# Kernel optimization log

Hardware: AMD Instinct MI355X
Metric: run time of the kernel (lower is better)

## Reference

```python
import jax, jax.numpy as jnp
import numpy as np

NHEADS = 4   # attention heads (search_cfg.nheads)
WS = 7       # spatial search window side -> WS*WS candidates per query
PS = 3       # patch size for distance computation (search_cfg.ps)
K = 16       # top-k neighbors kept (search_cfg.k)


def layer_norm_2d(vid, w, b, eps=1e-6):
    # LayerNorm over channel dim at every (t,h,w) location; vid (B,T,C,H,W)
    mu = vid.mean(axis=2, keepdims=True)
    var = vid.var(axis=2, keepdims=True)
    y = (vid - mu) / jnp.sqrt(var + eps)
    return y * w[None, None, :, None, None] + b[None, None, :, None, None]


def conv1x1(vid, w, b):
    # 1x1 ConvQKV projection: vid (B,T,C,H,W), w (O,C)
    return jnp.einsum('btchw,oc->btohw', vid, w) + b[None, None, :, None, None]


def box_sum(x, ps):
    # sum over centered ps x ps patch (zero pad); x (..., H, W)
    r = ps // 2
    H, W = x.shape[-2], x.shape[-1]
    xp = jnp.pad(x, [(0, 0)] * (x.ndim - 2) + [(r, r), (r, r)])
    out = jnp.zeros_like(x)
    ah, aw = x.ndim - 2, x.ndim - 1
    for dy in range(ps):
        for dx in range(ps):
            s = jax.lax.dynamic_slice_in_dim(xp, dy, H, ah)
            s = jax.lax.dynamic_slice_in_dim(s, dx, W, aw)
            out = out + s
    return out


def nl_search(q, k):
    # patch-based non-local search: q,k (B,T,HD,c,H,W)
    B, T, HD, c, H, W = q.shape
    r = WS // 2
    kp = jnp.pad(k, ((0, 0),) * 4 + ((r, r), (r, r)))  # zero pad = invalid candidates score ~0
    offs = jnp.stack(jnp.meshgrid(jnp.arange(WS), jnp.arange(WS), indexing='ij'), -1).reshape(-1, 2)

    @jax.checkpoint
    def step(carry, off):
        dy, dx = off[0], off[1]
        ksh = jax.lax.dynamic_slice(kp, (0, 0, 0, 0, dy, dx), (B, T, HD, c, H, W))
        s = (q * ksh).sum(axis=3)      # pixel inner products (B,T,HD,H,W)
        s = box_sum(s, PS)             # patch inner products
        return carry, s

    _, scores = jax.lax.scan(step, 0, offs)        # (WS*WS,B,T,HD,H,W)
    scores = jnp.moveaxis(scores, 0, -1)           # (B,T,HD,H,W,WS*WS)
    dists, inds = jax.lax.top_k(scores, K)         # top-k neighbors per query
    return dists, inds


def nl_stack(v, weights, inds):
    # gather the K selected neighbor values, weighted; v (B,T,HD,c,H,W)
    B, T, HD, c, H, W = v.shape
    r = WS // 2
    vp = jnp.pad(v, ((0, 0),) * 4 + ((r, r), (r, r)))
    Hp, Wp = H + 2 * r, W + 2 * r
    row = jnp.arange(H)[:, None, None] + inds // WS   # (B,T,HD,H,W,K)
    col = jnp.arange(W)[None, :, None] + inds % WS
    lin = (row * Wp + col).reshape(B, T, HD, 1, H * W * K)
    vf = vp.reshape(B, T, HD, c, Hp * Wp)
    g = jnp.take_along_axis(vf, jnp.broadcast_to(lin, (B, T, HD, c, H * W * K)), axis=-1)
    g = g.reshape(B, T, HD, c, H, W, K)
    g = g * weights[:, :, :, None]                    # weight each neighbor
    # -> (B*T, HD*c, K, H, W) stack for Conv3d projection
    return jnp.transpose(g, (0, 1, 2, 3, 6, 4, 5)).reshape(B * T, HD * c, K, H, W)


def proj3d(stack, w, b):
    # Conv3d(io_dim, io_dim, (K,3,3), stride=(K,1,1), pad=(0,1,1), groups=NHEADS)
    out = jax.lax.conv_general_dilated(
        stack, w, window_strides=(K, 1, 1),
        padding=((0, 0), (1, 1), (1, 1)),
        dimension_numbers=('NCDHW', 'OIDHW', 'NCDHW'),
        feature_group_count=NHEADS)
    return out[:, :, 0] + b[None, :, None, None]


def setup_inputs() -> dict:
    key = jax.random.key(0)
    ks = jax.random.split(key, 8)
    B, T, C, H, W = 1, 4, 128, 96, 96
    sc = 1.0 / np.sqrt(C)
    inp = {
        'vid': jax.random.normal(ks[0], (B, T, C, H, W), jnp.float32),
        'ln_w': jnp.ones((C,), jnp.float32),
        'ln_b': jnp.zeros((C,), jnp.float32),
        'wq': jax.random.normal(ks[1], (C, C), jnp.float32) * sc,
        'bq': jnp.zeros((C,), jnp.float32),
        'wk': jax.random.normal(ks[2], (C, C), jnp.float32) * sc,
        'bk': jnp.zeros((C,), jnp.float32),
        'wv': jax.random.normal(ks[3], (C, C), jnp.float32) * sc,
        'bv': jnp.zeros((C,), jnp.float32),
        'proj_w': jax.random.normal(ks[4], (C, C // NHEADS, K, 3, 3), jnp.float32) * 0.02,
        'proj_b': jnp.zeros((C,), jnp.float32),
    }
    return inp


def reference(vid, ln_w, ln_b, wq, bq, wk, bk, wv, bv, proj_w, proj_b):
    B, T, C, H, W = vid.shape
    x = layer_norm_2d(vid, ln_w, ln_b)
    q = conv1x1(x, wq, bq)
    k = conv1x1(x, wk, bk)
    v = conv1x1(x, wv, bv)
    hd = lambda t: t.reshape(B, T, NHEADS, C // NHEADS, H, W)
    q, k, v = hd(q), hd(k), hd(v)
    dists, inds = nl_search(q, k)                 # k-NN search
    weights = jax.nn.softmax(dists, axis=-1)      # normalize over K
    stack = nl_stack(v, weights, inds)            # neighbor stacking
    out = proj3d(stack, proj_w, proj_b)           # conv projection collapses K
    return out.reshape(B, T, C, H, W)
```

## Files before the change

kernel.cpp:

```cpp
#include <hip/hip_runtime.h>


typedef float  f32x4  __attribute__((ext_vector_type(4)));
typedef __bf16 bf16x8 __attribute__((ext_vector_type(8)));
typedef __bf16 bf16x4 __attribute__((ext_vector_type(4)));

__device__ __forceinline__ float dpp_shr1(float x) {
  return __int_as_float(__builtin_amdgcn_update_dpp(0, __float_as_int(x), 0x111, 0xf, 0xf, false));
}
__device__ __forceinline__ float dpp_shl1(float x) {
  return __int_as_float(__builtin_amdgcn_update_dpp(0, __float_as_int(x), 0x101, 0xf, 0xf, false));
}

__global__ __launch_bounds__(256) void prep_kernel(
    const float* __restrict__ wq, const float* __restrict__ wk, const float* __restrict__ wv,
    const float* __restrict__ pw, float* __restrict__ Wt, __bf16* __restrict__ pwt) {
  int idx = blockIdx.x * 256 + threadIdx.x;
  const int NPW = 4 * 16 * 9 * 32 * 32;
  if (idx < NPW) {
    int i  = idx & 31;
    int ol = (idx >> 5) & 31;
    int d  = (idx >> 10) % 9;
    int r  = (idx >> 10) / 9;
    int kd = r & 15;
    int g  = r >> 4;
    int o  = g * 32 + ol;
    pwt[idx] = (__bf16)pw[((o * 32 + i) * 16 + kd) * 9 + d];
  } else {
    int widx = idx - NPW;
    if (widx < 128 * 384) {
      int o = widx % 384;
      int c = widx / 384;
      const float* __restrict__ src = (o < 128) ? wq : (o < 256 ? wk : wv);
      Wt[widx] = src[(o & 127) * 128 + c];
    }
  }
}

__global__ __launch_bounds__(64) void ln_stats_kernel(
    const float* __restrict__ vid, float* __restrict__ mu, float* __restrict__ rs) {
  int pix = blockIdx.x * 64 + threadIdx.x;
  int f = blockIdx.y;
  const float* __restrict__ vp = vid + (size_t)f * 128 * 9216 + pix;
  float s = 0.f, s2 = 0.f;
  #pragma unroll 8
  for (int c = 0; c < 128; ++c) { float x = vp[(size_t)c * 9216]; s += x; s2 += x * x; }
  float m_ = s * (1.f / 128.f);
  float v_ = fmaxf(s2 * (1.f / 128.f) - m_ * m_, 0.f);
  mu[f * 9216 + pix] = m_;
  rs[f * 9216 + pix] = rsqrtf(v_ + 1e-6f);
}

__global__ __launch_bounds__(512) void qkv_gemm_kernel(
    const float* __restrict__ vid, const float* __restrict__ mu, const float* __restrict__ rs,
    const float* __restrict__ lnw, const float* __restrict__ lnb,
    const float* __restrict__ Wt, const float* __restrict__ bq, const float* __restrict__ bk,
    const float* __restrict__ bv, float* __restrict__ qb, float* __restrict__ kb,
    __bf16* __restrict__ vbbf) {
  __shared__ __align__(16) float Xs[32][128];
  __shared__ __align__(16) float Ws[32][128];
  __shared__ float muL[128], rsL[128], lwS[128], lbS[128];
  int tid = threadIdx.x;
  int mt = blockIdx.y;
  int N0 = blockIdx.x * 128;
  int f  = mt / 72;
  int pf = (mt % 72) * 128;

  if (tid < 128) {
    muL[tid] = mu[f * 9216 + pf + tid];
    rsL[tid] = rs[f * 9216 + pf + tid];
  } else if (tid < 256) {
    int t2 = tid - 128;
    lwS[t2] = lnw[t2];
    lbS[t2] = lnb[t2];
  }

  int tx = tid & 15, ty = tid >> 4;
  int m0 = ty * 4;
  int sm = tid & 127;
  int sk = tid >> 7;
  float acc[4][8];
  #pragma unroll
  for (int a = 0; a < 4; ++a)
    #pragma unroll
    for (int b = 0; b < 8; ++b) acc[a][b] = 0.f;

  const size_t vbase = (size_t)f * 128 * 9216 + pf;
  float xr[8], wr[8];

  #pragma unroll
  for (int it = 0; it < 8; ++it) {
    int kk = sk + 4 * it;
    xr[it] = vid[vbase + (size_t)kk * 9216 + sm];
    wr[it] = Wt[(size_t)kk * 384 + N0 + sm];
  }
  __syncthreads();
  #pragma unroll
  for (int it = 0; it < 8; ++it) {
    int kk = sk + 4 * it;
    Xs[kk][sm] = (xr[it] - muL[sm]) * rsL[sm] * lwS[kk] + lbS[kk];
    Ws[kk][sm] = wr[it];
  }
  __syncthreads();

  for (int kc = 0; kc < 4; ++kc) {
    if (kc < 3) {
      #pragma unroll
      for (int it = 0; it < 8; ++it) {
        int kk = sk + 4 * it;
        int c = (kc + 1) * 32 + kk;
        xr[it] = vid[vbase + (size_t)c * 9216 + sm];
        wr[it] = Wt[(size_t)c * 384 + N0 + sm];
      }
    }
    #pragma unroll 4
    for (int kk = 0; kk < 32; ++kk) {
      float xa[4], wa[8];
      *(float4*)&xa[0] = *(const float4*)&Xs[kk][m0];
      *(float4*)&wa[0] = *(const float4*)&Ws[kk][tx * 4];
      *(float4*)&wa[4] = *(const float4*)&Ws[kk][64 + tx * 4];
      #pragma unroll
      for (int a = 0; a < 4; ++a)
        #pragma unroll
        for (int b = 0; b < 8; ++b)
          acc[a][b] = fmaf(xa[a], wa[b], acc[a][b]);
    }
    if (kc < 3) {
      __syncthreads();
      #pragma unroll
      for (int it = 0; it < 8; ++it) {
        int kk = sk + 4 * it;
        int c = (kc + 1) * 32 + kk;
        Xs[kk][sm] = (xr[it] - muL[sm]) * rsL[sm] * lwS[c] + lbS[c];
        Ws[kk][sm] = wr[it];
      }
      __syncthreads();
    }
  }

  int sel = blockIdx.x;
  int nlo = tx * 4, nhi = 64 + tx * 4;
  int hlo = nlo >> 5, clo = nlo & 31;
  int hhi = nhi >> 5, chi = nhi & 31;
  const float* __restrict__ bias = (sel == 0) ? bq : (sel == 1 ? bk : bv);
  float4 blo = make_float4(bias[nlo], bias[nlo + 1], bias[nlo + 2], bias[nlo + 3]);
  float4 bhi = make_float4(bias[nhi], bias[nhi + 1], bias[nhi + 2], bias[nhi + 3]);
  size_t base_lo = (size_t)(f * 4 + hlo) * 9216 * 32 + clo;
  size_t base_hi = (size_t)(f * 4 + hhi) * 9216 * 32 + chi;
  if (sel < 2) {
    float* __restrict__ dst = (sel == 0) ? qb : kb;
    #pragma unroll
    for (int a = 0; a < 4; ++a) {
      size_t poff = (size_t)(pf + m0 + a) * 32;
      *(float4*)&dst[base_lo + poff] = make_float4(acc[a][0] + blo.x, acc[a][1] + blo.y,
                                                   acc[a][2] + blo.z, acc[a][3] + blo.w);
      *(float4*)&dst[base_hi + poff] = make_float4(acc[a][4] + bhi.x, acc[a][5] + bhi.y,
                                                   acc[a][6] + bhi.z, acc[a][7] + bhi.w);
    }
  } else {
    #pragma unroll
    for (int a = 0; a < 4; ++a) {
      size_t poff = (size_t)(pf + m0 + a) * 32;
      bf16x4 lo4, hi4;
      lo4[0] = (__bf16)(acc[a][0] + blo.x); lo4[1] = (__bf16)(acc[a][1] + blo.y);
      lo4[2] = (__bf16)(acc[a][2] + blo.z); lo4[3] = (__bf16)(acc[a][3] + blo.w);
      hi4[0] = (__bf16)(acc[a][4] + bhi.x); hi4[1] = (__bf16)(acc[a][5] + bhi.y);
      hi4[2] = (__bf16)(acc[a][6] + bhi.z); hi4[3] = (__bf16)(acc[a][7] + bhi.w);
      *(bf16x4*)&vbbf[base_lo + poff] = lo4;
      *(bf16x4*)&vbbf[base_hi + poff] = hi4;
    }
  }
}

__global__ __launch_bounds__(256, 3) void search_kernel(
    const float* __restrict__ qb, const float* __restrict__ kb,
    float* __restrict__ wgtb, int* __restrict__ indb) {
  __shared__ __align__(16) float klds[16 * 22 * 32];
  __shared__ float slds[7][256];
  int tid = threadIdx.x;
  int th = blockIdx.y;
  int tile = blockIdx.x;
  int iy0 = (tile / 7) * 14, ix0 = (tile % 7) * 14;
  const float* __restrict__ kbase = kb + (size_t)th * 9216 * 32;

  #pragma unroll
  for (int it = 0; it < 11; ++it) {
    int i = it * 256 + tid;
    int r = i / 176, rem = i % 176;
    int col = rem >> 3, c4 = rem & 7;
    int gy = iy0 - 4 + r, gx = ix0 - 4 + col;
    float4 val = make_float4(0.f, 0.f, 0.f, 0.f);
    if ((unsigned)gy < 96u && (unsigned)gx < 96u)
      val = *(const float4*)&kbase[(size_t)(gy * 96 + gx) * 32 + c4 * 4];
    int p = r * 22 + col;
    *(float4*)&klds[p * 32 + ((c4 ^ (p & 7)) << 2)] = val;
  }

  int sy = tid >> 4, sx = tid & 15;
  int qy = iy0 - 1 + sy, qx = ix0 - 1 + sx;
  bool qok = (unsigned)qy < 96u && (unsigned)qx < 96u;
  float4 qv[8];
  #pragma unroll
  for (int j = 0; j < 8; ++j) qv[j] = make_float4(0.f, 0.f, 0.f, 0.f);
  if (qok) {
    const float* __restrict__ qp = qb + ((size_t)th * 9216 + qy * 96 + qx) * 32;
    #pragma unroll
    for (int j = 0; j < 8; ++j) qv[j] = *(const float4*)&qp[j * 4];
  }
  bool inner = (sy >= 1) && (sy <= 14) && (sx >= 1) && (sx <= 14) && qok;

  float tv[16]; int tix[16];
  #pragma unroll
  for (int j = 0; j < 16; ++j) { tv[j] = -3.0e38f; tix[j] = 0; }
  __syncthreads();

  #pragma unroll 1
  for (int dy = 0; dy < 7; ++dy) {
    if (dy > 0) {
      if (tid < 176) {
        int col = tid >> 3, c4 = tid & 7;
        int r = dy + 15;
        int gy = iy0 - 4 + r, gx = ix0 - 4 + col;
        float4 val = make_float4(0.f, 0.f, 0.f, 0.f);
        if ((unsigned)gy < 96u && (unsigned)gx < 96u)
          val = *(const float4*)&kbase[(size_t)(gy * 96 + gx) * 32 + c4 * 4];
        int p = (r & 15) * 22 + col;
        *(float4*)&klds[p * 32 + ((c4 ^ (p & 7)) << 2)] = val;
      }
      __syncthreads();
    }
    float h[7];
    #pragma unroll
    for (int dx = 0; dx < 7; ++dx) {
      int p = ((sy + dy) & 15) * 22 + (sx + dx);
      const float* __restrict__ kp = &klds[p * 32];
      int sw = p & 7;
      float sdot = 0.f;
      #pragma unroll
      for (int j = 0; j < 8; ++j) {
        float4 kq = *(const float4*)&kp[(j ^ sw) << 2];
        sdot += qv[j].x * kq.x + qv[j].y * kq.y + qv[j].z * kq.z + qv[j].w * kq.w;
      }
      h[dx] = sdot + dpp_shr1(sdot) + dpp_shl1(sdot);
      slds[dx][tid] = h[dx];
    }
    __syncthreads();
    if (inner) {
      #pragma unroll
      for (int dx = 0; dx < 7; ++dx) {
        float sc = h[dx] + slds[dx][tid - 16] + slds[dx][tid + 16];
        int oi = dy * 7 + dx;
        float cv = sc; int ci = oi;
        #pragma unroll
        for (int j = 0; j < 16; ++j) {
          bool gt = cv > tv[j];
          float mx = fmaxf(tv[j], cv);
          float mn = fminf(tv[j], cv);
          int nt = gt ? ci : tix[j];
          ci = gt ? tix[j] : ci;
          tv[j] = mx; cv = mn; tix[j] = nt;
        }
      }
    }
  }

  if (inner) {
    float mx = tv[0];
    float e[16], ssum = 0.f;
    #pragma unroll
    for (int j = 0; j < 16; ++j) { e[j] = __expf(tv[j] - mx); ssum += e[j]; }
    float inv = 1.f / ssum;
    size_t base = ((size_t)th * 9216 + qy * 96 + qx) * 16;
    #pragma unroll
    for (int j = 0; j < 4; ++j) {
      *(float4*)&wgtb[base + j * 4] =
          make_float4(e[j*4] * inv, e[j*4+1] * inv, e[j*4+2] * inv, e[j*4+3] * inv);
      *(int4*)&indb[base + j * 4] = make_int4(tix[j*4], tix[j*4+1], tix[j*4+2], tix[j*4+3]);
    }
  }
}

#define STAGE_A(BUF, VR, WC) do {                                              \
  if (gact) {                                                                  \
    __bf16 tmp_[32];                                                           \
    _Pragma("unroll")                                                          \
    for (int wv_ = 0; wv_ < 4; ++wv_) {                                        \
      unsigned uu_[4] = {(unsigned)VR[wv_].x, (unsigned)VR[wv_].y,             \
                         (unsigned)VR[wv_].z, (unsigned)VR[wv_].w};            \
      _Pragma("unroll")                                                        \
      for (int j2_ = 0; j2_ < 4; ++j2_) {                                      \
        float lo_ = __uint_as_float(uu_[j2_] << 16);                           \
        float hi_ = __uint_as_float(uu_[j2_] & 0xffff0000u);                   \
        tmp_[wv_ * 8 + j2_ * 2]     = (__bf16)(lo_ * (WC));                    \
        tmp_[wv_ * 8 + j2_ * 2 + 1] = (__bf16)(hi_ * (WC));                    \
      }                                                                        \
    }                                                                          \
    __bf16* dst_ = &(BUF)[tid * 32];                                           \
    int sela_ = (tid >> 1) & 3;                                                \
    *(int4*)&dst_[(0 ^ sela_) << 3] = *(const int4*)&tmp_[0];                  \
    *(int4*)&dst_[(1 ^ sela_) << 3] = *(const int4*)&tmp_[8];                  \
    *(int4*)&dst_[(2 ^ sela_) << 3] = *(const int4*)&tmp_[16];                 \
    *(int4*)&dst_[(3 ^ sela_) << 3] = *(const int4*)&tmp_[24];                 \
  }                                                                            \
} while (0)

#define STAGE_B(BUF, KD) do {                                                  \
  const __bf16* __restrict__ bsrc_ = pwt + (size_t)(g * 16 + (KD)) * 9216;     \
  _Pragma("unroll")                                                            \
  for (int itb_ = 0; itb_ < 3; ++itb_) {                                       \
    int i_ = itb_ * 512 + tid;                                                 \
    if (i_ < 1152) {                                                           \
      int row_ = i_ >> 2, c_ = i_ & 3;                                         \
      *(int4*)&(BUF)[row_ * 32 + ((c_ ^ ((row_ >> 1) & 3)) << 3)] =            \
          *(const int4*)&bsrc_[row_ * 32 + c_ * 8];                            \
    }                                                                          \
  }                                                                            \
} while (0)

#define GATHER(VR, WC, IND, W) do {                                            \
  int ind_ = (IND);                                                            \
  VR[0] = VR[1] = VR[2] = VR[3] = make_int4(0, 0, 0, 0);                       \
  if (inb) {                                                                   \
    int ny_ = gy + ind_ / 7 - 3, nx_ = gx + ind_ % 7 - 3;                      \
    if ((unsigned)ny_ < 96u && (unsigned)nx_ < 96u) {                          \
      const int4* __restrict__ vp_ =                                           \
          (const int4*)(vbase + (size_t)(ny_ * 96 + nx_) * 32);                \
      VR[0] = vp_[0]; VR[1] = vp_[1]; VR[2] = vp_[2]; VR[3] = vp_[3];          \
    }                                                                          \
  }                                                                            \
  WC = (W);                                                                    \
} while (0)

#define MFMA_PHASE(AB, BB) do {                                                \
  _Pragma("unroll")                                                            \
  for (int dx2_ = 0; dx2_ < 3; ++dx2_) {                                       \
    bf16x8 a_[4];                                                              \
    _Pragma("unroll")                                                          \
    for (int r_ = 0; r_ < 4; ++r_) {                                           \
      int p_ = (wid * 2 + r_) * 18 + lr + dx2_;                                \
      a_[r_] = *(const bf16x8*)&(AB)[p_ * 32 + ((kg ^ ((p_ >> 1) & 3)) << 3)]; \
    }                                                                          \
    _Pragma("unroll")                                                          \
    for (int dy2_ = 0; dy2_ < 3; ++dy2_) {                                     \
      int d_ = dy2_ * 3 + dx2_;                                                \
      bf16x8 b0_ = *(const bf16x8*)&(BB)[(d_ * 32 + lr) * 32 + bswz];          \
      bf16x8 b1_ = *(const bf16x8*)&(BB)[(d_ * 32 + 16 + lr) * 32 + bswz];     \
      acc[0][0] = __builtin_amdgcn_mfma_f32_16x16x32_bf16(a_[dy2_],     b0_, acc[0][0], 0, 0, 0); \
      acc[0][1] = __builtin_amdgcn_mfma_f32_16x16x32_bf16(a_[dy2_],     b1_, acc[0][1], 0, 0, 0); \
      acc[1][0] = __builtin_amdgcn_mfma_f32_16x16x32_bf16(a_[dy2_ + 1], b0_, acc[1][0], 0, 0, 0); \
      acc[1][1] = __builtin_amdgcn_mfma_f32_16x16x32_bf16(a_[dy2_ + 1], b1_, acc[1][1], 0, 0, 0); \
    }                                                                          \
  }                                                                            \
} while (0)

__global__ __launch_bounds__(512) void proj_kernel(
    const __bf16* __restrict__ vb, const float* __restrict__ wgtb, const int* __restrict__ indb,
    const __bf16* __restrict__ pwt, const float* __restrict__ pb, float* __restrict__ outp) {
  __shared__ __align__(16) __bf16 Albuf[2][324 * 32];
  __shared__ __align__(16) __bf16 Blbuf[2][288 * 32];
  int tid = threadIdx.x;
  int bid = blockIdx.x;
  int wg = (bid & 7) * 72 + (bid >> 3);
  int th = wg / 36;
  int tile = wg % 36;
  int g = th & 3;
  int ty0 = (tile / 6) * 16, tx0 = (tile % 6) * 16;
  int lane = tid & 63, wid = tid >> 6;
  int kg = lane >> 4, lr = lane & 15;
  int bswz = (kg ^ ((lr >> 1) & 3)) << 3;

  bool gact = tid < 324;
  int ry = tid / 18, rx = tid % 18;
  int gy = ty0 - 1 + ry, gx = tx0 - 1 + rx;
  bool inb = gact && (unsigned)gy < 96u && (unsigned)gx < 96u;
  const __bf16* __restrict__ vbase = vb + (size_t)th * 9216 * 32;
  size_t pxoff = inb ? (size_t)(gy * 96 + gx) : 0;
  const int*   __restrict__ ibase = indb + ((size_t)th * 9216 + pxoff) * 16;
  const float* __restrict__ wbase = wgtb + ((size_t)th * 9216 + pxoff) * 16;

  f32x4 acc[2][2];
  acc[0][0] = (f32x4)(0.0f); acc[0][1] = (f32x4)(0.0f);
  acc[1][0] = (f32x4)(0.0f); acc[1][1] = (f32x4)(0.0f);

  int4 iw_i = make_int4(0, 0, 0, 0);
  float4 iw_w = make_float4(0.f, 0.f, 0.f, 0.f);
  int4 vr0[4], vr1[4];
  float wc0 = 0.f, wc1 = 0.f;

  if (inb) {
    iw_i = *(const int4*)&ibase[0];
    iw_w = *(const float4*)&wbase[0];
  }
  GATHER(vr0, wc0, iw_i.x, iw_w.x);
  STAGE_A(Albuf[0], vr0, wc0);
  STAGE_B(Blbuf[0], 0);
  GATHER(vr1, wc1, iw_i.y, iw_w.y);
  __syncthreads();

  #pragma unroll 1
  for (int kq = 0; kq < 4; ++kq) {
    int k4 = kq * 4;
    STAGE_A(Albuf[1], vr1, wc1);
    STAGE_B(Blbuf[1], k4 + 1);
    GATHER(vr0, wc0, iw_i.z, iw_w.z);
    MFMA_PHASE(Albuf[0], Blbuf[0]);
    __syncthreads();
    STAGE_A(Albuf[0], vr0, wc0);
    STAGE_B(Blbuf[0], k4 + 2);
    GATHER(vr1, wc1, iw_i.w, iw_w.w);
    MFMA_PHASE(Albuf[1], Blbuf[1]);
    __syncthreads();
    STAGE_A(Albuf[1], vr1, wc1);
    STAGE_B(Blbuf[1], k4 + 3);
    if (kq < 3) {
      if (inb) {
        iw_i = *(const int4*)&ibase[k4 + 4];
        iw_w = *(const float4*)&wbase[k4 + 4];
      }
      GATHER(vr0, wc0, iw_i.x, iw_w.x);
    }
    MFMA_PHASE(Albuf[0], Blbuf[0]);
    __syncthreads();
    if (kq < 3) {
      STAGE_A(Albuf[0], vr0, wc0);
      STAGE_B(Blbuf[0], k4 + 4);
      GATHER(vr1, wc1, iw_i.y, iw_w.y);
    }
    MFMA_PHASE(Albuf[1], Blbuf[1]);
    __syncthreads();
  }

  int x0 = tx0 + kg * 4;
  int f = th >> 2;
  #pragma unroll
  for (int mt = 0; mt < 2; ++mt) {
    int y = ty0 + wid * 2 + mt;
    #pragma unroll
    for (int nt = 0; nt < 2; ++nt) {
      int o = g * 32 + nt * 16 + lr;
      float bias = pb[o];
      float4 res = make_float4(acc[mt][nt][0] + bias, acc[mt][nt][1] + bias,
                               acc[mt][nt][2] + bias, acc[mt][nt][3] + bias);
      *(float4*)&outp[(size_t)(f * 128 + o) * 9216 + y * 96 + x0] = res;
    }
  }
}

extern "C" void kernel_launch(void* const* d_in, const int* in_sizes, int n_in,
                              void* d_out, int out_size, void* d_ws, size_t ws_size,
                              hipStream_t stream) {
  const float* vid = (const float*)d_in[0];
  const float* lnw = (const float*)d_in[1];
  const float* lnb = (const float*)d_in[2];
  const float* wq  = (const float*)d_in[3];
  const float* bq  = (const float*)d_in[4];
  const float* wk  = (const float*)d_in[5];
  const float* bk  = (const float*)d_in[6];
  const float* wv_ = (const float*)d_in[7];
  const float* bv  = (const float*)d_in[8];
  const float* pw  = (const float*)d_in[9];
  const float* pb  = (const float*)d_in[10];
  float* outp = (float*)d_out;

  const size_t SZ_T  = (size_t)16 * 9216 * 32 * 4;
  const size_t SZ_TB = (size_t)16 * 9216 * 32 * 2;
  const size_t SZ_W  = (size_t)16 * 9216 * 16 * 4;
  const size_t SZ_WT = 128 * 384 * 4;
  const size_t SZ_PW = (size_t)4 * 16 * 9 * 32 * 32 * 2;
  const size_t SZ_MU = (size_t)4 * 9216 * 4;

  char* p = (char*)d_ws;
  float* qb = (float*)p;        p += SZ_T;
  float* kb = (float*)p;        p += SZ_T;
  __bf16* vbbf = (__bf16*)p;    p += SZ_TB;
  float* wgtb = (float*)p;      p += SZ_W;
  int*   indb = (int*)p;        p += SZ_W;
  float* Wt = (float*)p;        p += SZ_WT;
  __bf16* pwt = (__bf16*)p;     p += SZ_PW;
  float* mu = (float*)p;        p += SZ_MU;
  float* rs = (float*)p;

  prep_kernel<<<2496, 256, 0, stream>>>(wq, wk, wv_, pw, Wt, pwt);
  ln_stats_kernel<<<dim3(144, 4), 64, 0, stream>>>(vid, mu, rs);
  qkv_gemm_kernel<<<dim3(3, 288), 512, 0, stream>>>(vid, mu, rs, lnw, lnb, Wt, bq, bk, bv,
                                                    qb, kb, vbbf);
  search_kernel<<<dim3(49, 16), 256, 0, stream>>>(qb, kb, wgtb, indb);
  proj_kernel<<<576, 512, 0, stream>>>(vbbf, wgtb, indb, pwt, pb, outp);
}
```

Measured before the change: 209.9 us.

## Compute V projection with bf16 MFMA from a precomputed normalized bf16 input

The V third of the fp32 QKV GEMM is split out. A new kernel writes the layer-normalized input as channel-contiguous bf16, and a new kernel computes V with bf16 MFMA instructions using swizzled LDS tiles. Q and K stay on the existing fp32 GEMM, which now runs two column blocks instead of three. This moves V onto matrix cores, at the cost of two extra launches, an extra bf16 buffer written and read through global memory, and lower precision in the V inputs.

```diff
diff --git a/kernel.cpp b/kernel.cpp
--- a/kernel.cpp
+++ b/kernel.cpp
@@ -3,7 +3,6 @@
 
 typedef float  f32x4  __attribute__((ext_vector_type(4)));
 typedef __bf16 bf16x8 __attribute__((ext_vector_type(8)));
-typedef __bf16 bf16x4 __attribute__((ext_vector_type(4)));
 
 __device__ __forceinline__ float dpp_shr1(float x) {
   return __int_as_float(__builtin_amdgcn_update_dpp(0, __float_as_int(x), 0x111, 0xf, 0xf, false));
@@ -14,7 +13,8 @@
 
 __global__ __launch_bounds__(256) void prep_kernel(
     const float* __restrict__ wq, const float* __restrict__ wk, const float* __restrict__ wv,
-    const float* __restrict__ pw, float* __restrict__ Wt, __bf16* __restrict__ pwt) {
+    const float* __restrict__ pw, float* __restrict__ Wt, __bf16* __restrict__ pwt,
+    __bf16* __restrict__ wvh) {
   int idx = blockIdx.x * 256 + threadIdx.x;
   const int NPW = 4 * 16 * 9 * 32 * 32;
   if (idx < NPW) {
@@ -26,14 +26,15 @@
     int g  = r >> 4;
     int o  = g * 32 + ol;
     pwt[idx] = (__bf16)pw[((o * 32 + i) * 16 + kd) * 9 + d];
+  } else if (idx < NPW + 128 * 384) {
+    int widx = idx - NPW;
+    int o = widx % 384;
+    int c = widx / 384;
+    const float* __restrict__ src = (o < 128) ? wq : (o < 256 ? wk : wv);
+    Wt[widx] = src[(o & 127) * 128 + c];
   } else {
-    int widx = idx - NPW;
-    if (widx < 128 * 384) {
-      int o = widx % 384;
-      int c = widx / 384;
-      const float* __restrict__ src = (o < 128) ? wq : (o < 256 ? wk : wv);
-      Wt[widx] = src[(o & 127) * 128 + c];
-    }
+    int vidx = idx - NPW - 128 * 384;
+    if (vidx < 128 * 128) wvh[vidx] = (__bf16)wv[vidx];
   }
 }
 
@@ -51,12 +52,47 @@
   rs[f * 9216 + pix] = rsqrtf(v_ + 1e-6f);
 }
 
-__global__ __launch_bounds__(512) void qkv_gemm_kernel(
+__global__ __launch_bounds__(256) void xbf_kernel(
+    const float* __restrict__ vid, const float* __restrict__ mu, const float* __restrict__ rs,
+    const float* __restrict__ lnw, const float* __restrict__ lnb, __bf16* __restrict__ xbf) {
+  __shared__ __align__(16) __bf16 tile[128 * 128];
+  __shared__ float muL[128], rsL[128], lwS[128], lbS[128];
+  int t = threadIdx.x;
+  int pf = blockIdx.x * 128;
+  int f = blockIdx.y;
+  if (t < 128) { muL[t] = mu[f * 9216 + pf + t]; rsL[t] = rs[f * 9216 + pf + t]; }
+  else { lwS[t - 128] = lnw[t - 128]; lbS[t - 128] = lnb[t - 128]; }
+  __syncthreads();
+  #pragma unroll 4
+  for (int it = 0; it < 16; ++it) {
+    int idx = it * 256 + t;
+    int c = idx >> 5, p4 = idx & 31;
+    float4 v = *(const float4*)&vid[((size_t)(f * 128 + c)) * 9216 + pf + p4 * 4];
+    float xs[4] = {v.x, v.y, v.z, v.w};
+    #pragma unroll
+    for (int i = 0; i < 4; ++i) {
+      int pix = p4 * 4 + i;
+      float xn = (xs[i] - muL[pix]) * rsL[pix] * lwS[c] + lbS[c];
+      int cp = c ^ (((pix >> 2) & 7) << 3);
+      tile[pix * 128 + cp] = (__bf16)xn;
+    }
+  }
+  __syncthreads();
+  int pix = t >> 1, half = t & 1;
+  __bf16* __restrict__ dst = xbf + ((size_t)(f * 9216) + pf + pix) * 128 + half * 64;
+  #pragma unroll
+  for (int cc = 0; cc < 8; ++cc) {
+    int chunk = half * 8 + cc;
+    int cs = chunk ^ ((pix >> 2) & 7);
+    *(int4*)&dst[cc * 8] = *(const int4*)&tile[pix * 128 + cs * 8];
+  }
+}
+
+__global__ __launch_bounds__(512) void qk_gemm_kernel(
     const float* __restrict__ vid, const float* __restrict__ mu, const float* __restrict__ rs,
     const float* __restrict__ lnw, const float* __restrict__ lnb,
     const float* __restrict__ Wt, const float* __restrict__ bq, const float* __restrict__ bk,
-    const float* __restrict__ bv, float* __restrict__ qb, float* __restrict__ kb,
-    __bf16* __restrict__ vbbf) {
+    float* __restrict__ qb, float* __restrict__ kb) {
   __shared__ __align__(16) float Xs[32][128];
   __shared__ __align__(16) float Ws[32][128];
   __shared__ float muL[128], rsL[128], lwS[128], lbS[128];
@@ -142,32 +178,91 @@
   int nlo = tx * 4, nhi = 64 + tx * 4;
   int hlo = nlo >> 5, clo = nlo & 31;
   int hhi = nhi >> 5, chi = nhi & 31;
-  const float* __restrict__ bias = (sel == 0) ? bq : (sel == 1 ? bk : bv);
+  const float* __restrict__ bias = (sel == 0) ? bq : bk;
+  float* __restrict__ dst = (sel == 0) ? qb : kb;
   float4 blo = make_float4(bias[nlo], bias[nlo + 1], bias[nlo + 2], bias[nlo + 3]);
   float4 bhi = make_float4(bias[nhi], bias[nhi + 1], bias[nhi + 2], bias[nhi + 3]);
   size_t base_lo = (size_t)(f * 4 + hlo) * 9216 * 32 + clo;
   size_t base_hi = (size_t)(f * 4 + hhi) * 9216 * 32 + chi;
-  if (sel < 2) {
-    float* __restrict__ dst = (sel == 0) ? qb : kb;
-    #pragma unroll
-    for (int a = 0; a < 4; ++a) {
-      size_t poff = (size_t)(pf + m0 + a) * 32;
-      *(float4*)&dst[base_lo + poff] = make_float4(acc[a][0] + blo.x, acc[a][1] + blo.y,
-                                                   acc[a][2] + blo.z, acc[a][3] + blo.w);
-      *(float4*)&dst[base_hi + poff] = make_float4(acc[a][4] + bhi.x, acc[a][5] + bhi.y,
-                                                   acc[a][6] + bhi.z, acc[a][7] + bhi.w);
-    }
-  } else {
-    #pragma unroll
-    for (int a = 0; a < 4; ++a) {
-      size_t poff = (size_t)(pf + m0 + a) * 32;
-      bf16x4 lo4, hi4;
-      lo4[0] = (__bf16)(acc[a][0] + blo.x); lo4[1] = (__bf16)(acc[a][1] + blo.y);
-      lo4[2] = (__bf16)(acc[a][2] + blo.z); lo4[3] = (__bf16)(acc[a][3] + blo.w);
-      hi4[0] = (__bf16)(acc[a][4] + bhi.x); hi4[1] = (__bf16)(acc[a][5] + bhi.y);
-      hi4[2] = (__bf16)(acc[a][6] + bhi.z); hi4[3] = (__bf16)(acc[a][7] + bhi.w);
-      *(bf16x4*)&vbbf[base_lo + poff] = lo4;
-      *(bf16x4*)&vbbf[base_hi + poff] = hi4;
+  #pragma unroll
+  for (int a = 0; a < 4; ++a) {
+    size_t poff = (size_t)(pf + m0 + a) * 32;
+    *(float4*)&dst[base_lo + poff] = make_float4(acc[a][0] + blo.x, acc[a][1] + blo.y,
+                                                 acc[a][2] + blo.z, acc[a][3] + blo.w);
+    *(float4*)&dst[base_hi + poff] = make_float4(acc[a][4] + bhi.x, acc[a][5] + bhi.y,
+                                                 acc[a][6] + bhi.z, acc[a][7] + bhi.w);
+  }
+}
+
+__global__ __launch_bounds__(256) void vmfma_kernel(
+    const __bf16* __restrict__ xbf, const __bf16* __restrict__ wvh,
+    const float* __restrict__ bv, __bf16* __restrict__ vbbf) {
+  __shared__ __align__(16) __bf16 XL[64 * 128];
+  __shared__ __align__(16) __bf16 WL[128 * 128];
+  int t = threadIdx.x;
+  int bid = blockIdx.x;
+  int f = bid / 144;
+  int pf = (bid % 144) * 64;
+
+  #pragma unroll
+  for (int i = 0; i < 4; ++i) {
+    int idx = i * 256 + t;
+    int pix = idx >> 4, ck = idx & 15;
+    int4 val = *(const int4*)&xbf[((size_t)(f * 9216) + pf + pix) * 128 + ck * 8];
+    *(int4*)&XL[pix * 128 + ((ck ^ (pix & 7)) << 3)] = val;
+  }
+  #pragma unroll
+  for (int i = 0; i < 8; ++i) {
+    int idx = i * 256 + t;
+    int o = idx >> 4, ck = idx & 15;
+    int4 val = *(const int4*)&wvh[o * 128 + ck * 8];
+    *(int4*)&WL[o * 128 + ((ck ^ (o & 7)) << 3)] = val;
+  }
+  __syncthreads();
+
+  int lane = t & 63, w = t >> 6;
+  int wm = w >> 1, wn = w & 1;
+  int kg = lane >> 4, lr = lane & 15;
+  f32x4 acc[2][4];
+  #pragma unroll
+  for (int mf = 0; mf < 2; ++mf)
+    #pragma unroll
+    for (int nf = 0; nf < 4; ++nf) acc[mf][nf] = (f32x4)(0.0f);
+
+  #pragma unroll
+  for (int kc = 0; kc < 4; ++kc) {
+    int ck = kc * 4 + kg;
+    bf16x8 a[2], b[4];
+    #pragma unroll
+    for (int mf = 0; mf < 2; ++mf) {
+      int pix = wm * 32 + mf * 16 + lr;
+      a[mf] = *(const bf16x8*)&XL[pix * 128 + ((ck ^ (pix & 7)) << 3)];
+    }
+    #pragma unroll
+    for (int nf = 0; nf < 4; ++nf) {
+      int o = wn * 64 + nf * 16 + lr;
+      b[nf] = *(const bf16x8*)&WL[o * 128 + ((ck ^ (o & 7)) << 3)];
+    }
+    #pragma unroll
+    for (int mf = 0; mf < 2; ++mf)
+      #pragma unroll
+      for (int nf = 0; nf < 4; ++nf)
+        acc[mf][nf] = __builtin_amdgcn_mfma_f32_16x16x32_bf16(a[mf], b[nf], acc[mf][nf], 0, 0, 0);
+  }
+
+  #pragma unroll
+  for (int mf = 0; mf < 2; ++mf) {
+    #pragma unroll
+    for (int nf = 0; nf < 4; ++nf) {
+      int o = wn * 64 + nf * 16 + lr;
+      int head = o >> 5, c = o & 31;
+      float bias = bv[o];
+      #pragma unroll
+      for (int j = 0; j < 4; ++j) {
+        int pix = wm * 32 + mf * 16 + kg * 4 + j;
+        vbbf[((size_t)((f * 4 + head) * 9216) + pf + pix) * 32 + c] =
+            (__bf16)(acc[mf][nf][j] + bias);
+      }
     }
   }
 }
@@ -468,6 +563,8 @@
   const size_t SZ_WT = 128 * 384 * 4;
   const size_t SZ_PW = (size_t)4 * 16 * 9 * 32 * 32 * 2;
   const size_t SZ_MU = (size_t)4 * 9216 * 4;
+  const size_t SZ_XB = (size_t)4 * 9216 * 128 * 2;
+  const size_t SZ_WV = 128 * 128 * 2;
 
   char* p = (char*)d_ws;
   float* qb = (float*)p;        p += SZ_T;
@@ -478,12 +575,15 @@
   float* Wt = (float*)p;        p += SZ_WT;
   __bf16* pwt = (__bf16*)p;     p += SZ_PW;
   float* mu = (float*)p;        p += SZ_MU;
-  float* rs = (float*)p;
-
-  prep_kernel<<<2496, 256, 0, stream>>>(wq, wk, wv_, pw, Wt, pwt);
+  float* rs = (float*)p;        p += SZ_MU;
+  __bf16* xbf = (__bf16*)p;     p += SZ_XB;
+  __bf16* wvh = (__bf16*)p;
+
+  prep_kernel<<<2560, 256, 0, stream>>>(wq, wk, wv_, pw, Wt, pwt, wvh);
   ln_stats_kernel<<<dim3(144, 4), 64, 0, stream>>>(vid, mu, rs);
-  qkv_gemm_kernel<<<dim3(3, 288), 512, 0, stream>>>(vid, mu, rs, lnw, lnb, Wt, bq, bk, bv,
-                                                    qb, kb, vbbf);
+  xbf_kernel<<<dim3(72, 4), 256, 0, stream>>>(vid, mu, rs, lnw, lnb, xbf);
+  qk_gemm_kernel<<<dim3(2, 288), 512, 0, stream>>>(vid, mu, rs, lnw, lnb, Wt, bq, bk, qb, kb);
+  vmfma_kernel<<<576, 256, 0, stream>>>(xbf, wvh, bv, vbbf);
   search_kernel<<<dim3(49, 16), 256, 0, stream>>>(qb, kb, wgtb, indb);
   proj_kernel<<<576, 512, 0, stream>>>(vbbf, wgtb, indb, pwt, pb, outp);
 }
```

Result: no change. 213.7 us (+1.8%).
